# Performance work log

Measured on AMD Instinct MI355X. Metric: run time of the kernel, lower is better.

Reference implementation:

```python
import jax, jax.numpy as jnp
import numpy as np

B, S, E, H = 2, 2048, 1024, 16
D = E // H  # head_dim = 64
NEG = -1e9


def setup_inputs() -> dict:
    key = jax.random.key(0)
    ks = jax.random.split(key, 12)
    def xavier(k, shape):
        fan_in, fan_out = shape[1], shape[0]
        lim = jnp.sqrt(6.0 / (fan_in + fan_out))
        return jax.random.uniform(k, shape, jnp.float32, -lim, lim)
    inp = {
        'Q_input': jax.random.normal(ks[0], (B, S, E), jnp.float32),
        'K_input': jax.random.normal(ks[1], (B, S, E), jnp.float32),
        'V_input': jax.random.normal(ks[2], (B, S, E), jnp.float32),
        'causal_mask': jnp.where(jnp.tril(jnp.ones((S, S), bool)), 0.0, NEG).astype(jnp.float32),
        'padding_mask': jnp.zeros((B, S), bool),
        'W_q': xavier(ks[3], (E, E)), 'b_q': jnp.zeros((E,), jnp.float32),
        'W_k': xavier(ks[4], (E, E)), 'b_k': jnp.zeros((E,), jnp.float32),
        'W_v': xavier(ks[5], (E, E)), 'b_v': jnp.zeros((E,), jnp.float32),
        'W_o': xavier(ks[6], (E, E)), 'b_o': jnp.zeros((E,), jnp.float32),
    }
    return inp


def reference(Q_input, K_input, V_input, causal_mask, padding_mask,
              W_q, b_q, W_k, b_k, W_v, b_v, W_o, b_o):
    b = Q_input.shape[0]
    # linear proj (torch convention: x @ W.T + b), split into heads -> [B,H,S,D]
    def proj(x, W, bias):
        y = x @ W.T + bias
        return y.reshape(b, -1, H, D).transpose(0, 2, 1, 3)
    Q = proj(Q_input, W_q, b_q)
    K = proj(K_input, W_k, b_k)
    V = proj(V_input, W_v, b_v)
    scale = 1.0 / jnp.sqrt(jnp.float32(D))
    scores = jnp.einsum('bhqd,bhkd->bhqk', Q, K) * scale  # [B,H,Sq,Sk]
    scores = jnp.where(padding_mask[:, None, None, :], NEG, scores)
    scores = scores + causal_mask  # broadcasts [Sq,Sk]
    attn = jax.nn.softmax(scores, axis=-1)
    ctx = jnp.einsum('bhqk,bhkd->bhqd', attn, V)
    ctx = ctx.transpose(0, 2, 1, 3).reshape(b, -1, E)
    return ctx @ W_o.T + b_o
```

## Files before the change

### kernel.cpp

```cpp
#include <hip/hip_runtime.h>
#include <hip/hip_bf16.h>

#define B_ 2
#define S_ 2048
#define E_ 1024
#define H_ 16
#define D_ 64

typedef __bf16 bf16x8 __attribute__((ext_vector_type(8)));
typedef __bf16 bf16x4 __attribute__((ext_vector_type(4)));
typedef float f32x4 __attribute__((ext_vector_type(4)));

#define MFMA16(a, b, c) __builtin_amdgcn_mfma_f32_16x16x32_bf16(a, b, c, 0, 0, 0)

__device__ __forceinline__ void cp16(const void* g, void* l) {
  __builtin_amdgcn_global_load_lds((const __attribute__((address_space(1))) void*)g,
                                   (__attribute__((address_space(3))) void*)l, 16, 0, 0);
}

__device__ __forceinline__ unsigned pack2(float a, float b) {
  unsigned short ua = __builtin_bit_cast(unsigned short, (__bf16)a);
  unsigned short ub = __builtin_bit_cast(unsigned short, (__bf16)b);
  return (unsigned)ua | ((unsigned)ub << 16);
}

__global__ __launch_bounds__(256) void cast_all(
    const float* __restrict__ w0, const float* __restrict__ w1,
    const float* __restrict__ w2, const float* __restrict__ w3,
    const float* __restrict__ x0, const float* __restrict__ x1,
    const float* __restrict__ x2,
    __bf16* __restrict__ dW, __bf16* __restrict__ dX)
{
  const float* srcs[7] = {w0, w1, w2, w3, x0, x1, x2};
  const int y = blockIdx.y;
  const bool isW = y < 4;
  const size_t n = isW ? (size_t)E_ * E_ : (size_t)B_ * S_ * E_;
  size_t i = ((size_t)blockIdx.x * 256 + threadIdx.x) * 8;
  if (i >= n) return;
  const float* src = srcs[y];
  __bf16* dst = isW ? dW + (size_t)y * E_ * E_ : dX + (size_t)(y - 4) * B_ * S_ * E_;
  f32x4 a = *(const f32x4*)(src + i);
  f32x4 b = *(const f32x4*)(src + i + 4);
  bf16x8 o;
#pragma unroll
  for (int j = 0; j < 4; ++j) { o[j] = (__bf16)a[j]; o[j + 4] = (__bf16)b[j]; }
  *(bf16x8*)(dst + i) = o;
}

__global__ __launch_bounds__(256) void gemm_qkv(
    const __bf16* __restrict__ Xb, const __bf16* __restrict__ Wc,
    const float* __restrict__ bq, const float* __restrict__ bk,
    const float* __restrict__ bv, __bf16* __restrict__ Proj)
{
  __shared__ __bf16 As[2][128 * 32];
  __shared__ __bf16 Bs[2][128 * 32];

  const int tid  = threadIdx.x;
  const int wave = tid >> 6, lane = tid & 63;
  const int l15  = lane & 15, quad = lane >> 4;
  const int wr = wave >> 1, wc = wave & 1;
  const int m0 = blockIdx.x * 128;
  const int wid = blockIdx.y >> 3;
  const int n0 = (blockIdx.y & 7) * 128;

  const __bf16* X   = Xb + (size_t)wid * B_ * S_ * E_;
  const float* bias = wid == 0 ? bq : (wid == 1 ? bk : bv);
  const __bf16* W   = Wc + (size_t)wid * E_ * E_;
  __bf16* Out       = Proj + (size_t)wid * B_ * S_ * E_;

  auto stage = [&](int k0, int bi) {
#pragma unroll
    for (int i = 0; i < 2; ++i) {
      int c = i * 256 + tid;
      int row = c >> 2, cg = c & 3;
      cp16(X + (size_t)(m0 + row) * E_ + k0 + cg * 8,
           (char*)&As[bi][0] + i * 4096 + wave * 1024);
    }
#pragma unroll
    for (int i = 0; i < 2; ++i) {
      int c = i * 256 + tid;
      int row = c >> 2, cg = c & 3;
      cp16(W + (size_t)(n0 + row) * E_ + k0 + cg * 8,
           (char*)&Bs[bi][0] + i * 4096 + wave * 1024);
    }
  };

  f32x4 acc[4][4];
#pragma unroll
  for (int i = 0; i < 4; ++i)
#pragma unroll
    for (int j = 0; j < 4; ++j) acc[i][j] = (f32x4){0, 0, 0, 0};

  stage(0, 0);
  int cur = 0;
  for (int k0 = 0; k0 < E_; k0 += 32) {
    if (k0 + 32 < E_) {
      stage(k0 + 32, cur ^ 1);
      asm volatile("s_waitcnt vmcnt(4)" ::: "memory");
    } else {
      asm volatile("s_waitcnt vmcnt(0)" ::: "memory");
    }
    __builtin_amdgcn_s_barrier();

    bf16x8 af[4], bfr[4];
#pragma unroll
    for (int ms = 0; ms < 4; ++ms) {
      int row = wr * 64 + ms * 16 + l15;
      af[ms] = *(const bf16x8*)((const char*)&As[cur][0] + row * 64 + quad * 16);
    }
#pragma unroll
    for (int ns = 0; ns < 4; ++ns) {
      int row = wc * 64 + ns * 16 + l15;
      bfr[ns] = *(const bf16x8*)((const char*)&Bs[cur][0] + row * 64 + quad * 16);
    }
    __builtin_amdgcn_s_setprio(1);
#pragma unroll
    for (int ms = 0; ms < 4; ++ms)
#pragma unroll
      for (int ns = 0; ns < 4; ++ns)
        acc[ms][ns] = MFMA16(af[ms], bfr[ns], acc[ms][ns]);
    __builtin_amdgcn_s_setprio(0);

    asm volatile("" ::: "memory");
    __builtin_amdgcn_s_barrier();
    asm volatile("" ::: "memory");
    cur ^= 1;
  }

#pragma unroll
  for (int ns = 0; ns < 4; ++ns) {
    int n = n0 + wc * 64 + ns * 16 + l15;
    float bv_ = bias[n];
#pragma unroll
    for (int ms = 0; ms < 4; ++ms)
#pragma unroll
      for (int r = 0; r < 4; ++r) {
        int m = m0 + wr * 64 + ms * 16 + quad * 4 + r;
        Out[(size_t)m * E_ + n] = (__bf16)(acc[ms][ns][r] + bv_);
      }
  }
}

__global__ __launch_bounds__(256) void gemm_out(
    const __bf16* __restrict__ X, const __bf16* __restrict__ W,
    const float* __restrict__ bias, float* __restrict__ out)
{
  __shared__ __bf16 As[2][64 * 32];
  __shared__ __bf16 Bs[2][128 * 32];

  const int tid  = threadIdx.x;
  const int wave = tid >> 6, lane = tid & 63;
  const int l15  = lane & 15, quad = lane >> 4;
  const int wr = wave >> 1, wc = wave & 1;
  const int m0 = blockIdx.x * 64;
  const int n0 = blockIdx.y * 128;

  auto stage = [&](int k0, int bi) {
    {
      int row = tid >> 2, cg = tid & 3;
      cp16(X + (size_t)(m0 + row) * E_ + k0 + cg * 8,
           (char*)&As[bi][0] + wave * 1024);
    }
#pragma unroll
    for (int i = 0; i < 2; ++i) {
      int c = i * 256 + tid;
      int row = c >> 2, cg = c & 3;
      cp16(W + (size_t)(n0 + row) * E_ + k0 + cg * 8,
           (char*)&Bs[bi][0] + i * 4096 + wave * 1024);
    }
  };

  f32x4 acc[2][4];
#pragma unroll
  for (int i = 0; i < 2; ++i)
#pragma unroll
    for (int j = 0; j < 4; ++j) acc[i][j] = (f32x4){0, 0, 0, 0};

  stage(0, 0);
  int cur = 0;
  for (int k0 = 0; k0 < E_; k0 += 32) {
    if (k0 + 32 < E_) {
      stage(k0 + 32, cur ^ 1);
      asm volatile("s_waitcnt vmcnt(3)" ::: "memory");
    } else {
      asm volatile("s_waitcnt vmcnt(0)" ::: "memory");
    }
    __builtin_amdgcn_s_barrier();

    bf16x8 af[2], bfr[4];
#pragma unroll
    for (int ms = 0; ms < 2; ++ms) {
      int row = wr * 32 + ms * 16 + l15;
      af[ms] = *(const bf16x8*)((const char*)&As[cur][0] + row * 64 + quad * 16);
    }
#pragma unroll
    for (int ns = 0; ns < 4; ++ns) {
      int row = wc * 64 + ns * 16 + l15;
      bfr[ns] = *(const bf16x8*)((const char*)&Bs[cur][0] + row * 64 + quad * 16);
    }
    __builtin_amdgcn_s_setprio(1);
#pragma unroll
    for (int ms = 0; ms < 2; ++ms)
#pragma unroll
      for (int ns = 0; ns < 4; ++ns)
        acc[ms][ns] = MFMA16(af[ms], bfr[ns], acc[ms][ns]);
    __builtin_amdgcn_s_setprio(0);

    asm volatile("" ::: "memory");
    __builtin_amdgcn_s_barrier();
    asm volatile("" ::: "memory");
    cur ^= 1;
  }

#pragma unroll
  for (int ns = 0; ns < 4; ++ns) {
    int n = n0 + wc * 64 + ns * 16 + l15;
    float bv_ = bias[n];
#pragma unroll
    for (int ms = 0; ms < 2; ++ms)
#pragma unroll
      for (int r = 0; r < 4; ++r) {
        int m = m0 + wr * 32 + ms * 16 + quad * 4 + r;
        out[(size_t)m * E_ + n] = acc[ms][ns][r] + bv_;
      }
  }
}

__global__ __launch_bounds__(64) void transpose_v(
    const __bf16* __restrict__ Vp, __bf16* __restrict__ Vt)
{
  const int lane = threadIdx.x;
  const int b = blockIdx.y >> 4;
  const int h = blockIdx.y & 15;
  const int s0 = blockIdx.x * 64 + (lane & 7) * 8;
  const int d0 = (lane >> 3) * 8;

  bf16x8 in[8];
#pragma unroll
  for (int j = 0; j < 8; ++j)
    in[j] = *(const bf16x8*)&Vp[(((size_t)b * S_ + s0 + j) * H_ + h) * D_ + d0];
#pragma unroll
  for (int i = 0; i < 8; ++i) {
    bf16x8 t;
#pragma unroll
    for (int j = 0; j < 8; ++j) t[j] = in[j][i];
    *(bf16x8*)&Vt[(((size_t)b * H_ + h) * D_ + d0 + i) * S_ + s0] = t;
  }
}

__global__ __launch_bounds__(256, 4) void attn_fwd(
    const __bf16* __restrict__ Qp, const __bf16* __restrict__ Kp,
    const __bf16* __restrict__ Vt, __bf16* __restrict__ Ctx)
{
  const int tid  = threadIdx.x;
  const int wave = tid >> 6;
  const int lane = tid & 63;
  const int l15  = lane & 15;
  const int quad = lane >> 4;
  const int x = blockIdx.x;
  const int y = blockIdx.y;
  const int b = y >> 4;
  const int h = y & 15;

  __shared__ __bf16 Ksh[2][64 * 64];
  __shared__ __bf16 Vsh[2][64 * 64];

  const __bf16* Khb = Kp + (size_t)b * S_ * E_ + h * 64;
  const __bf16* Vhb = Vt + ((size_t)b * H_ + h) * D_ * S_;

  auto stage = [&](int c, int bi) {
    const int kb0 = c * 64;
#pragma unroll
    for (int i = 0; i < 2; ++i) {
      int cc = i * 256 + tid;
      int key = cc >> 3, p = cc & 7;
      int pg = p ^ (key & 7);
      cp16(Khb + (size_t)(kb0 + key) * E_ + pg * 8,
           (char*)&Ksh[bi][0] + i * 4096 + wave * 1024);
    }
#pragma unroll
    for (int i = 0; i < 2; ++i) {
      int cc = i * 256 + tid;
      int d = cc >> 3, kp = cc & 7;
      int kpg = kp ^ (d & 7);
      cp16(Vhb + (size_t)d * S_ + kb0 + kpg * 8,
           (char*)&Vsh[bi][0] + i * 4096 + wave * 1024);
    }
  };

  const int hb = quad >> 1;
  const int s0l = (2 * (quad & 1)) * 16 + l15;
  const int s1l = s0l + 16;
  const float esc = 0.18033688011f;

  for (int ti = 0; ti < 2; ++ti) {
    const int t = ti ? 31 - x : x;
    const int q0 = t * 64;
    const int wq0 = q0 + wave * 16;

    bf16x8 qa[2];
#pragma unroll
    for (int kk = 0; kk < 2; ++kk) {
      bf16x8 q = *(const bf16x8*)&Qp[(size_t)(b * S_ + wq0 + l15) * E_ +
                                     h * 64 + kk * 32 + quad * 8];
#pragma unroll
      for (int j = 0; j < 8; ++j) q[j] = (__bf16)((float)q[j] * esc);
      qa[kk] = q;
    }

    f32x4 o[4];
    float rs = 0.f;
#pragma unroll
    for (int ds = 0; ds < 4; ++ds) o[ds] = (f32x4){0, 0, 0, 0};

    const int nch = t + 1;

    stage(0, 0);
    int cur = 0;
    for (int c = 0; c < nch; ++c) {
      if (c + 1 < nch) {
        stage(c + 1, cur ^ 1);
        asm volatile("s_waitcnt vmcnt(4)" ::: "memory");
      } else {
        asm volatile("s_waitcnt vmcnt(0)" ::: "memory");
      }
      __builtin_amdgcn_s_barrier();

      const int kb0 = c * 64;

      f32x4 sc[4];
      __builtin_amdgcn_s_setprio(1);
#pragma unroll
      for (int ks = 0; ks < 4; ++ks) {
        const char* Kpan = (const char*)&Ksh[cur][0];
        int row = ks * 16 + l15;
        bf16x8 kf0 = *(const bf16x8*)(Kpan + row * 128 + (((quad)     ^ (l15 & 7)) * 16));
        bf16x8 kf1 = *(const bf16x8*)(Kpan + row * 128 + (((4 + quad) ^ (l15 & 7)) * 16));
        f32x4 s = {0, 0, 0, 0};
        s = MFMA16(kf0, qa[0], s);
        s = MFMA16(kf1, qa[1], s);
        sc[ks] = s;
      }
      __builtin_amdgcn_s_setprio(0);

      unsigned pw[4][2];
      const bool msk = (kb0 + 63 > wq0);
      if (msk) {
#pragma unroll
        for (int ks = 0; ks < 4; ++ks) {
          float p[4];
#pragma unroll
          for (int r = 0; r < 4; ++r) {
            float e = exp2f(sc[ks][r]);
            if (kb0 + ks * 16 + quad * 4 + r > wq0 + l15) e = 0.f;
            rs += e;
            p[r] = e;
          }
          pw[ks][0] = pack2(p[0], p[1]);
          pw[ks][1] = pack2(p[2], p[3]);
        }
      } else {
#pragma unroll
        for (int ks = 0; ks < 4; ++ks) {
          float p[4];
#pragma unroll
          for (int r = 0; r < 4; ++r) {
            float e = exp2f(sc[ks][r]);
            rs += e;
            p[r] = e;
          }
          pw[ks][0] = pack2(p[0], p[1]);
          pw[ks][1] = pack2(p[2], p[3]);
        }
      }

      bf16x8 pf[2];
#pragma unroll
      for (int kk = 0; kk < 2; ++kk) {
        unsigned w[4];
#pragma unroll
        for (int wi = 0; wi < 4; ++wi) {
          int src = (wi & 2) ? s1l : s0l;
          unsigned g0 = __shfl(pw[2 * kk + 0][wi & 1], src, 64);
          unsigned g1 = __shfl(pw[2 * kk + 1][wi & 1], src, 64);
          w[wi] = hb ? g1 : g0;
        }
        union { unsigned u[4]; bf16x8 v; } cvt;
        cvt.u[0] = w[0]; cvt.u[1] = w[1]; cvt.u[2] = w[2]; cvt.u[3] = w[3];
        pf[kk] = cvt.v;
      }

      __builtin_amdgcn_s_setprio(1);
#pragma unroll
      for (int ds = 0; ds < 4; ++ds) {
        int row = ds * 16 + l15;
#pragma unroll
        for (int kk = 0; kk < 2; ++kk) {
          const char* Vpan = (const char*)&Vsh[cur][0];
          bf16x8 vf = *(const bf16x8*)(Vpan + row * 128 +
                                       (((kk * 4 + quad) ^ (l15 & 7)) * 16));
          o[ds] = MFMA16(pf[kk], vf, o[ds]);
        }
      }
      __builtin_amdgcn_s_setprio(0);

      asm volatile("" ::: "memory");
      __builtin_amdgcn_s_barrier();
      asm volatile("" ::: "memory");
      cur ^= 1;
    }

    float s = rs;
    s += __shfl_xor(s, 16, 64);
    s += __shfl_xor(s, 32, 64);
    float inv = 1.f / s;

#pragma unroll
    for (int r = 0; r < 4; ++r) {
      float invr = __shfl(inv, quad * 4 + r, 64);
      size_t base = (size_t)(b * S_ + wq0 + quad * 4 + r) * E_ + h * 64;
#pragma unroll
      for (int ds = 0; ds < 4; ++ds)
        Ctx[base + ds * 16 + l15] = (__bf16)(o[ds][r] * invr);
    }
  }
}

extern "C" void kernel_launch(void* const* d_in, const int* in_sizes, int n_in,
                              void* d_out, int out_size, void* d_ws, size_t ws_size,
                              hipStream_t stream)
{
  const float* Qin = (const float*)d_in[0];
  const float* Kin = (const float*)d_in[1];
  const float* Vin = (const float*)d_in[2];
  const float* Wq = (const float*)d_in[5];
  const float* bq = (const float*)d_in[6];
  const float* Wk = (const float*)d_in[7];
  const float* bk = (const float*)d_in[8];
  const float* Wv = (const float*)d_in[9];
  const float* bv = (const float*)d_in[10];
  const float* Wo = (const float*)d_in[11];
  const float* bo = (const float*)d_in[12];

  __bf16* ws = (__bf16*)d_ws;
  const size_t WSZ = (size_t)E_ * E_;
  const size_t T   = (size_t)B_ * S_ * E_;
  __bf16* Wc   = ws;
  __bf16* Proj = ws + 4 * WSZ;
  __bf16* Vt   = ws + 4 * WSZ + 3 * T;
  __bf16* Ctx  = ws + 4 * WSZ + 4 * T;
  __bf16* Xbf  = ws + 4 * WSZ + 5 * T;

  cast_all<<<dim3(2048, 7), 256, 0, stream>>>(Wq, Wk, Wv, Wo, Qin, Kin, Vin, Wc, Xbf);
  gemm_qkv<<<dim3(32, 24), 256, 0, stream>>>(Xbf, Wc, bq, bk, bv, Proj);
  transpose_v<<<dim3(S_ / 64, B_ * H_), 64, 0, stream>>>(Proj + 2 * T, Vt);
  attn_fwd<<<dim3(16, B_ * H_), 256, 0, stream>>>(Proj, Proj + T, Vt, Ctx);
  gemm_out<<<dim3(64, 8), 256, 0, stream>>>(Ctx, Wc + 3 * WSZ, bo, (float*)d_out);
}
```

Baseline: 244.2 us.

## Shrink attention blocks to 32 query rows, remap grid, use permlane swaps

The attention kernel now runs 128-thread blocks, each covering 32 query rows per tile, on a 1D grid of 1024 blocks. The grid index is remapped so neighbouring blocks spread across batch and head pairs, and the order of the two tiles each block handles alternates between halves of the grid for causal load balance. The shuffle-based P-matrix redistribution is replaced with v_permlane32/16_swap instructions to cut cross-lane shuffle cost. Smaller blocks add parallelism and balance, but each K/V chunk is now staged into shared memory for only half as many query rows, which raises redundant loads.

```diff
diff --git a/kernel.cpp b/kernel.cpp
--- a/kernel.cpp
+++ b/kernel.cpp
@@ -248,7 +248,7 @@
   }
 }
 
-__global__ __launch_bounds__(256, 4) void attn_fwd(
+__global__ __launch_bounds__(128, 2) void attn_fwd(
     const __bf16* __restrict__ Qp, const __bf16* __restrict__ Kp,
     const __bf16* __restrict__ Vt, __bf16* __restrict__ Ctx)
 {
@@ -257,10 +257,11 @@
   const int lane = tid & 63;
   const int l15  = lane & 15;
   const int quad = lane >> 4;
-  const int x = blockIdx.x;
-  const int y = blockIdx.y;
-  const int b = y >> 4;
-  const int h = y & 15;
+  const int id   = blockIdx.x;
+  const int bh   = (id & 7) * 4 + ((id >> 3) & 3);
+  const int pr   = id >> 5;
+  const int b    = bh >> 4;
+  const int h    = bh & 15;
 
   __shared__ __bf16 Ksh[2][64 * 64];
   __shared__ __bf16 Vsh[2][64 * 64];
@@ -271,32 +272,29 @@
   auto stage = [&](int c, int bi) {
     const int kb0 = c * 64;
 #pragma unroll
-    for (int i = 0; i < 2; ++i) {
-      int cc = i * 256 + tid;
+    for (int i = 0; i < 4; ++i) {
+      int cc = i * 128 + tid;
       int key = cc >> 3, p = cc & 7;
       int pg = p ^ (key & 7);
       cp16(Khb + (size_t)(kb0 + key) * E_ + pg * 8,
-           (char*)&Ksh[bi][0] + i * 4096 + wave * 1024);
-    }
-#pragma unroll
-    for (int i = 0; i < 2; ++i) {
-      int cc = i * 256 + tid;
+           (char*)&Ksh[bi][0] + i * 2048 + wave * 1024);
+    }
+#pragma unroll
+    for (int i = 0; i < 4; ++i) {
+      int cc = i * 128 + tid;
       int d = cc >> 3, kp = cc & 7;
       int kpg = kp ^ (d & 7);
       cp16(Vhb + (size_t)d * S_ + kb0 + kpg * 8,
-           (char*)&Vsh[bi][0] + i * 4096 + wave * 1024);
+           (char*)&Vsh[bi][0] + i * 2048 + wave * 1024);
     }
   };
 
-  const int hb = quad >> 1;
-  const int s0l = (2 * (quad & 1)) * 16 + l15;
-  const int s1l = s0l + 16;
   const float esc = 0.18033688011f;
+  const int swap_order = (id >> 8) & 1;
 
   for (int ti = 0; ti < 2; ++ti) {
-    const int t = ti ? 31 - x : x;
-    const int q0 = t * 64;
-    const int wq0 = q0 + wave * 16;
+    const int qb = (ti ^ swap_order) ? 63 - pr : pr;
+    const int wq0 = qb * 32 + wave * 16;
 
     bf16x8 qa[2];
 #pragma unroll
@@ -313,14 +311,14 @@
 #pragma unroll
     for (int ds = 0; ds < 4; ++ds) o[ds] = (f32x4){0, 0, 0, 0};
 
-    const int nch = t + 1;
+    const int nch = (qb >> 1) + 1;
 
     stage(0, 0);
     int cur = 0;
     for (int c = 0; c < nch; ++c) {
       if (c + 1 < nch) {
         stage(c + 1, cur ^ 1);
-        asm volatile("s_waitcnt vmcnt(4)" ::: "memory");
+        asm volatile("s_waitcnt vmcnt(8)" ::: "memory");
       } else {
         asm volatile("s_waitcnt vmcnt(0)" ::: "memory");
       }
@@ -377,16 +375,14 @@
       bf16x8 pf[2];
 #pragma unroll
       for (int kk = 0; kk < 2; ++kk) {
-        unsigned w[4];
-#pragma unroll
-        for (int wi = 0; wi < 4; ++wi) {
-          int src = (wi & 2) ? s1l : s0l;
-          unsigned g0 = __shfl(pw[2 * kk + 0][wi & 1], src, 64);
-          unsigned g1 = __shfl(pw[2 * kk + 1][wi & 1], src, 64);
-          w[wi] = hb ? g1 : g0;
-        }
+        unsigned a0 = pw[2 * kk + 0][0], a1 = pw[2 * kk + 0][1];
+        unsigned a2 = pw[2 * kk + 1][0], a3 = pw[2 * kk + 1][1];
+        asm("v_permlane32_swap_b32 %0, %1" : "+v"(a0), "+v"(a2));
+        asm("v_permlane32_swap_b32 %0, %1" : "+v"(a1), "+v"(a3));
+        asm("v_permlane16_swap_b32 %0, %1" : "+v"(a0), "+v"(a2));
+        asm("v_permlane16_swap_b32 %0, %1" : "+v"(a1), "+v"(a3));
         union { unsigned u[4]; bf16x8 v; } cvt;
-        cvt.u[0] = w[0]; cvt.u[1] = w[1]; cvt.u[2] = w[2]; cvt.u[3] = w[3];
+        cvt.u[0] = a0; cvt.u[1] = a1; cvt.u[2] = a2; cvt.u[3] = a3;
         pf[kk] = cvt.v;
       }
 
@@ -454,6 +450,6 @@
   cast_all<<<dim3(2048, 7), 256, 0, stream>>>(Wq, Wk, Wv, Wo, Qin, Kin, Vin, Wc, Xbf);
   gemm_qkv<<<dim3(32, 24), 256, 0, stream>>>(Xbf, Wc, bq, bk, bv, Proj);
   transpose_v<<<dim3(S_ / 64, B_ * H_), 64, 0, stream>>>(Proj + 2 * T, Vt);
-  attn_fwd<<<dim3(16, B_ * H_), 256, 0, stream>>>(Proj, Proj + T, Vt, Ctx);
+  attn_fwd<<<dim3(1024), 128, 0, stream>>>(Proj, Proj + T, Vt, Ctx);
   gemm_out<<<dim3(64, 8), 256, 0, stream>>>(Ctx, Wc + 3 * WSZ, bo, (float*)d_out);
 }
```

Measured after the change: 249.3 us. +2.1%, slower.
